# Kernel tuning notes

Hardware: AMD Instinct MI355X
Metric: run time of the kernel (lower is better)

Reference implementation:

```python
import jax, jax.numpy as jnp
import numpy as np

N = 8192
VOCAB = 32768
EMB = 128
HID = [128, 128]
NUM_CLASSES = 16
NUM_GRAPHS = 64


def setup_inputs() -> dict:
    key = jax.random.key(0)
    ks = jax.random.split(key, 10)
    x = jax.random.randint(ks[0], (N,), 0, VOCAB, dtype=jnp.int64 if jax.config.jax_enable_x64 else jnp.int32)
    m = jax.random.uniform(ks[1], (N, N), dtype=jnp.float32)  # dense weighted adjacency, positive degrees
    bm = (jnp.arange(N) * NUM_GRAPHS) // N  # sorted graph ids, every segment non-empty
    emb = jax.random.normal(ks[2], (VOCAB, EMB), dtype=jnp.float32)
    s1 = 1.0 / np.sqrt(EMB)
    w1 = jax.random.uniform(ks[3], (HID[0], EMB), jnp.float32, -s1, s1)
    b1 = jax.random.uniform(ks[4], (HID[0],), jnp.float32, -s1, s1)
    s2 = 1.0 / np.sqrt(HID[0])
    w2 = jax.random.uniform(ks[5], (HID[1], HID[0]), jnp.float32, -s2, s2)
    b2 = jax.random.uniform(ks[6], (HID[1],), jnp.float32, -s2, s2)
    sc = 1.0 / np.sqrt(HID[1])
    wc = jax.random.uniform(ks[7], (NUM_CLASSES, HID[1]), jnp.float32, -sc, sc)
    bc = jax.random.uniform(ks[8], (NUM_CLASSES,), jnp.float32, -sc, sc)
    return {"x": x, "m": m, "bm": bm, "emb": emb, "w1": w1, "b1": b1,
            "w2": w2, "b2": b2, "wc": wc, "bc": bc}


def _gcn_layer(h, m, w, b):
    # Linear -> ReLU (dropout=0 is identity)
    msg = jax.nn.relu(h @ w.T + b)
    row_deg = jnp.sum(m, axis=1, keepdims=True)   # (N,1)
    col_deg = jnp.sum(m, axis=0, keepdims=True)   # (1,N)
    deg = jnp.sqrt(row_deg) * jnp.sqrt(col_deg)   # rank-1 outer, same as mm(sqrt(rd), sqrt(cd))
    return (m / deg) @ msg                        # (N, out_dim)


def reference(x, m, bm, emb, w1, b1, w2, b2, wc, bc):
    h = emb[x]                                    # (N, EMB) embedding lookup
    h = _gcn_layer(h, m, w1, b1)
    h = _gcn_layer(h, m, w2, b2)
    pooled = jax.ops.segment_max(h, bm, num_segments=NUM_GRAPHS)  # (G, HID[-1]) max-pool per graph
    logits = pooled @ wc.T + bc                   # (G, NUM_CLASSES)
    return logits
```

## Files before the change

### kernel.cpp

```cpp
#include <hip/hip_runtime.h>
#include <stdint.h>


#define NN 8192
#define DH 128
#define NCLS 16
#define NGRAPH 64
#define SPLITK 8
#define KCHUNK (NN / SPLITK)

typedef float floatx4 __attribute__((ext_vector_type(4)));
typedef __bf16 bf16x8 __attribute__((ext_vector_type(8)));

__device__ __forceinline__ unsigned short f2bf_bits(float f) {
    union { float f; unsigned u; } v; v.f = f;
    unsigned u = v.u;
    u += 0x7fffu + ((u >> 16) & 1u);
    return (unsigned short)(u >> 16);
}

__device__ __forceinline__ void gload16(const void* g, void* l) {
    __builtin_amdgcn_global_load_lds(
        (const __attribute__((address_space(1))) void*)g,
        (__attribute__((address_space(3))) void*)l, 16, 0, 0);
}

__global__ __launch_bounds__(256) void k_zero(float* p, int n) {
    int i = blockIdx.x * 256 + threadIdx.x;
    if (i < n) p[i] = 0.f;
}

__global__ __launch_bounds__(256) void k_deg_cast(
    const float* __restrict__ m, unsigned short* __restrict__ mb,
    float* __restrict__ rd, float* __restrict__ cd)
{
    int rb = blockIdx.x >> 2;
    int cb = blockIdx.x & 3;
    int tid = threadIdx.x;
    int lane = tid & 63;
    int c = cb * 2048 + tid * 8;
    int r0 = rb * 32;
    float cs[8];
#pragma unroll
    for (int u = 0; u < 8; ++u) cs[u] = 0.f;
#pragma unroll 2
    for (int r = 0; r < 32; ++r) {
        int row = r0 + r;
        const float* p = m + (size_t)row * NN + c;
        float4 a = *(const float4*)p;
        float4 b = *(const float4*)(p + 4);
        cs[0] += a.x; cs[1] += a.y; cs[2] += a.z; cs[3] += a.w;
        cs[4] += b.x; cs[5] += b.y; cs[6] += b.z; cs[7] += b.w;
        float rs = ((a.x + a.y) + (a.z + a.w)) + ((b.x + b.y) + (b.z + b.w));
#pragma unroll
        for (int off = 1; off < 64; off <<= 1) rs += __shfl_xor(rs, off, 64);
        if (lane == 0) atomicAdd(&rd[row], rs);
        uint4 o;
        o.x = (unsigned)f2bf_bits(a.x) | ((unsigned)f2bf_bits(a.y) << 16);
        o.y = (unsigned)f2bf_bits(a.z) | ((unsigned)f2bf_bits(a.w) << 16);
        o.z = (unsigned)f2bf_bits(b.x) | ((unsigned)f2bf_bits(b.y) << 16);
        o.w = (unsigned)f2bf_bits(b.z) | ((unsigned)f2bf_bits(b.w) << 16);
        *(uint4*)(mb + (size_t)row * NN + c) = o;
    }
#pragma unroll
    for (int u = 0; u < 8; ++u) atomicAdd(&cd[c + u], cs[u]);
}

__global__ __launch_bounds__(256) void k_msg(
    const int* __restrict__ x, const float* __restrict__ emb,
    const float* __restrict__ part, const float* __restrict__ rdv,
    const float* __restrict__ w, const float* __restrict__ bias,
    const float* __restrict__ cdv, unsigned short* __restrict__ msgT,
    int layer)
{
    int tid = threadIdx.x;
    int wv = tid >> 6, lane = tid & 63;
    int quad = lane >> 4, r16 = lane & 15;
    int j = blockIdx.x * 64 + wv * 16 + r16;

    floatx4 acc[8];
#pragma unroll
    for (int t = 0; t < 8; ++t) acc[t] = (floatx4)0.f;

    const float* src;
    float presc = 1.f;
    if (layer == 1) {
        src = emb + (size_t)x[j] * DH;
    } else {
        src = part + (size_t)j * DH;
        presc = rsqrtf(rdv[j]);
    }

#pragma unroll
    for (int e0 = 0; e0 < DH; e0 += 32) {
        int ke = e0 + quad * 8;
        float v[8];
        if (layer == 1) {
            float4 a = *(const float4*)(src + ke);
            float4 b = *(const float4*)(src + ke + 4);
            v[0] = a.x; v[1] = a.y; v[2] = a.z; v[3] = a.w;
            v[4] = b.x; v[5] = b.y; v[6] = b.z; v[7] = b.w;
        } else {
#pragma unroll
            for (int u = 0; u < 8; ++u) v[u] = 0.f;
#pragma unroll
            for (int p2 = 0; p2 < SPLITK; ++p2) {
                const float* pp = src + (size_t)p2 * ((size_t)NN * DH) + ke;
                float4 a = *(const float4*)pp;
                float4 b = *(const float4*)(pp + 4);
                v[0] += a.x; v[1] += a.y; v[2] += a.z; v[3] += a.w;
                v[4] += b.x; v[5] += b.y; v[6] += b.z; v[7] += b.w;
            }
#pragma unroll
            for (int u = 0; u < 8; ++u) v[u] *= presc;
        }
        bf16x8 bf;
#pragma unroll
        for (int u = 0; u < 8; ++u) bf[u] = (__bf16)v[u];
#pragma unroll
        for (int t = 0; t < 8; ++t) {
            const float* wp = w + (size_t)(t * 16 + r16) * DH + ke;
            float4 wa = *(const float4*)wp;
            float4 wb = *(const float4*)(wp + 4);
            bf16x8 af;
            af[0] = (__bf16)wa.x; af[1] = (__bf16)wa.y; af[2] = (__bf16)wa.z; af[3] = (__bf16)wa.w;
            af[4] = (__bf16)wb.x; af[5] = (__bf16)wb.y; af[6] = (__bf16)wb.z; af[7] = (__bf16)wb.w;
            acc[t] = __builtin_amdgcn_mfma_f32_16x16x32_bf16(af, bf, acc[t], 0, 0, 0);
        }
    }
    float cs = rsqrtf(cdv[j]);
#pragma unroll
    for (int t = 0; t < 8; ++t) {
#pragma unroll
        for (int r = 0; r < 4; ++r) {
            int n = t * 16 + quad * 4 + r;
            float val = acc[t][r] + bias[n];
            val = fmaxf(val, 0.f) * cs;
            msgT[(size_t)n * NN + j] = f2bf_bits(val);
        }
    }
}

__global__ __launch_bounds__(256) void k_gemm(
    const unsigned short* __restrict__ A,
    const unsigned short* __restrict__ Bt,
    float* __restrict__ part)
{
    __shared__ unsigned short lA[128 * 32];
    __shared__ unsigned short lB[128 * 32];
    int mblk = blockIdx.x & 63;
    int kp = blockIdx.x >> 6;
    int tid = threadIdx.x;
    int wv = tid >> 6, lane = tid & 63;
    int quad = lane >> 4, r16 = lane & 15;
    int wm = wv >> 1, wn = wv & 1;
    size_t mbase = (size_t)mblk * 128;
    int kbase = kp * KCHUNK;

    floatx4 acc[4][4];
#pragma unroll
    for (int mi = 0; mi < 4; ++mi)
#pragma unroll
        for (int ni = 0; ni < 4; ++ni) acc[mi][ni] = (floatx4)0.f;

    int srow = lane >> 2;
    int kq = lane & 3;
    const unsigned short* gA = A + (mbase + wv * 32 + srow) * (size_t)NN + kbase + kq * 8;
    const unsigned short* gB = Bt + (size_t)(wv * 32 + srow) * NN + kbase + kq * 8;
    char* lAw = (char*)lA + wv * 2048;
    char* lBw = (char*)lB + wv * 2048;

    for (int it = 0; it < KCHUNK / 32; ++it) {
        gload16(gA, lAw);
        gload16(gA + (size_t)16 * NN, lAw + 1024);
        gload16(gB, lBw);
        gload16(gB + (size_t)16 * NN, lBw + 1024);
        __syncthreads();
        bf16x8 af[4], bf[4];
#pragma unroll
        for (int mi = 0; mi < 4; ++mi)
            af[mi] = *(const bf16x8*)((const char*)lA + ((wm * 64 + mi * 16 + r16) * 64 + quad * 16));
#pragma unroll
        for (int ni = 0; ni < 4; ++ni)
            bf[ni] = *(const bf16x8*)((const char*)lB + ((wn * 64 + ni * 16 + r16) * 64 + quad * 16));
#pragma unroll
        for (int mi = 0; mi < 4; ++mi)
#pragma unroll
            for (int ni = 0; ni < 4; ++ni)
                acc[mi][ni] = __builtin_amdgcn_mfma_f32_16x16x32_bf16(af[mi], bf[ni], acc[mi][ni], 0, 0, 0);
        __syncthreads();
        gA += 32; gB += 32;
    }

    float* outp = part + (size_t)kp * ((size_t)NN * DH);
#pragma unroll
    for (int mi = 0; mi < 4; ++mi) {
#pragma unroll
        for (int r = 0; r < 4; ++r) {
            size_t i = mbase + wm * 64 + mi * 16 + quad * 4 + r;
            float* op = outp + i * DH + wn * 64 + r16;
#pragma unroll
            for (int ni = 0; ni < 4; ++ni) op[ni * 16] = acc[mi][ni][r];
        }
    }
}

__global__ __launch_bounds__(256) void k_pool(
    const float* __restrict__ part, const float* __restrict__ rdv,
    const float* __restrict__ wc, const float* __restrict__ bc,
    float* __restrict__ out)
{
    __shared__ float red[256];
    __shared__ float pooled[128];
    int g = blockIdx.x;
    int tid = threadIdx.x;
    int c = tid & 127;
    int half = tid >> 7;
    float mx = -1e30f;
    for (int r = 0; r < 64; ++r) {
        int i = g * 128 + half * 64 + r;
        float s = 0.f;
#pragma unroll
        for (int p = 0; p < SPLITK; ++p)
            s += part[(size_t)p * ((size_t)NN * DH) + (size_t)i * DH + c];
        s *= rsqrtf(rdv[i]);
        mx = fmaxf(mx, s);
    }
    red[tid] = mx;
    __syncthreads();
    if (half == 0) pooled[c] = fmaxf(red[c], red[c + 128]);
    __syncthreads();
    if (tid < NCLS) {
        float a = bc[tid];
        const float* wr = wc + tid * 128;
#pragma unroll 8
        for (int k = 0; k < 128; ++k) a += pooled[k] * wr[k];
        out[g * NCLS + tid] = a;
    }
}

extern "C" void kernel_launch(void* const* d_in, const int* in_sizes, int n_in,
                              void* d_out, int out_size, void* d_ws, size_t ws_size,
                              hipStream_t stream)
{
    const int*   x   = (const int*)  d_in[0];
    const float* m   = (const float*)d_in[1];
    const float* emb = (const float*)d_in[3];
    const float* w1  = (const float*)d_in[4];
    const float* b1  = (const float*)d_in[5];
    const float* w2  = (const float*)d_in[6];
    const float* b2  = (const float*)d_in[7];
    const float* wc  = (const float*)d_in[8];
    const float* bc  = (const float*)d_in[9];
    float* out = (float*)d_out;

    char* ws = (char*)d_ws;
    unsigned short* mb = (unsigned short*)ws;
    float* rd  = (float*)(ws + (size_t)134217728);
    float* cd  = rd + NN;
    unsigned short* msgT = (unsigned short*)(cd + NN);
    float* part = (float*)((char*)msgT + (size_t)2 * NN * DH);

    k_zero<<<(2 * NN + 255) / 256, 256, 0, stream>>>(rd, 2 * NN);
    k_deg_cast<<<1024, 256, 0, stream>>>(m, mb, rd, cd);
    k_msg<<<NN / 64, 256, 0, stream>>>(x, emb, nullptr, nullptr, w1, b1, cd, msgT, 1);
    k_gemm<<<64 * SPLITK, 256, 0, stream>>>(mb, msgT, part);
    k_msg<<<NN / 64, 256, 0, stream>>>(nullptr, nullptr, part, rd, w2, b2, cd, msgT, 2);
    k_gemm<<<64 * SPLITK, 256, 0, stream>>>(mb, msgT, part);
    k_pool<<<NGRAPH, 256, 0, stream>>>(part, rd, wc, bc, out);
}
```

Before: 580.9 us.

## Split degree/cast kernel, drop LDS staging in GEMM, parallelize pooling

Replaces the fused degree+cast kernel, which used atomics, with three kernels: a row-per-wave cast that computes row sums directly, a column partial-sum pass over the bf16 copy, and a final column reduction. This removes the atomics and the zeroing kernel. The GEMM drops LDS staging and loads MFMA fragments straight from global memory, double-buffered in registers. Pooling is spread over 8x more blocks, with a separate small classify kernel. The extra pass over the 128MB bf16 matrix for column sums and the uncoalesced direct-global GEMM loads may add memory traffic, and column degrees are now summed from bf16-rounded values.

```diff
diff --git a/kernel.cpp b/kernel.cpp
--- a/kernel.cpp
+++ b/kernel.cpp
@@ -8,62 +8,75 @@
 #define NGRAPH 64
 #define SPLITK 8
 #define KCHUNK (NN / SPLITK)
+#define CDSLICE 256
 
 typedef float floatx4 __attribute__((ext_vector_type(4)));
 typedef __bf16 bf16x8 __attribute__((ext_vector_type(8)));
 
-__device__ __forceinline__ unsigned short f2bf_bits(float f) {
+__device__ __forceinline__ unsigned f2bf_bits(float f) {
     union { float f; unsigned u; } v; v.f = f;
     unsigned u = v.u;
     u += 0x7fffu + ((u >> 16) & 1u);
-    return (unsigned short)(u >> 16);
-}
-
-__device__ __forceinline__ void gload16(const void* g, void* l) {
-    __builtin_amdgcn_global_load_lds(
-        (const __attribute__((address_space(1))) void*)g,
-        (__attribute__((address_space(3))) void*)l, 16, 0, 0);
-}
-
-__global__ __launch_bounds__(256) void k_zero(float* p, int n) {
-    int i = blockIdx.x * 256 + threadIdx.x;
-    if (i < n) p[i] = 0.f;
-}
-
-__global__ __launch_bounds__(256) void k_deg_cast(
+    return u >> 16;
+}
+__device__ __forceinline__ float bf2f(unsigned bits16) {
+    union { unsigned u; float f; } v; v.u = bits16 << 16; return v.f;
+}
+
+__global__ __launch_bounds__(256) void k_cast(
     const float* __restrict__ m, unsigned short* __restrict__ mb,
-    float* __restrict__ rd, float* __restrict__ cd)
-{
-    int rb = blockIdx.x >> 2;
-    int cb = blockIdx.x & 3;
-    int tid = threadIdx.x;
-    int lane = tid & 63;
-    int c = cb * 2048 + tid * 8;
-    int r0 = rb * 32;
-    float cs[8];
-#pragma unroll
-    for (int u = 0; u < 8; ++u) cs[u] = 0.f;
-#pragma unroll 2
+    float* __restrict__ rd)
+{
+    int wv = threadIdx.x >> 6, lane = threadIdx.x & 63;
+    int row = blockIdx.x * 4 + wv;
+    const float* src = m + (size_t)row * NN;
+    unsigned short* dst = mb + (size_t)row * NN;
+    float rsum = 0.f;
+#pragma unroll 4
+    for (int it = 0; it < 32; ++it) {
+        int c = it * 256 + lane * 4;
+        float4 a = *(const float4*)(src + c);
+        rsum += (a.x + a.y) + (a.z + a.w);
+        uint2 o;
+        o.x = f2bf_bits(a.x) | (f2bf_bits(a.y) << 16);
+        o.y = f2bf_bits(a.z) | (f2bf_bits(a.w) << 16);
+        *(uint2*)(dst + c) = o;
+    }
+#pragma unroll
+    for (int off = 1; off < 64; off <<= 1) rsum += __shfl_xor(rsum, off, 64);
+    if (lane == 0) rd[row] = rsum;
+}
+
+__global__ __launch_bounds__(256) void k_cd(
+    const unsigned short* __restrict__ mb, float* __restrict__ cdpart)
+{
+    int cb = blockIdx.x & 3, rb = blockIdx.x >> 2;
+    int c = cb * 2048 + threadIdx.x * 8;
+    const unsigned short* p = mb + (size_t)rb * 32 * NN + c;
+    float s[8];
+#pragma unroll
+    for (int u = 0; u < 8; ++u) s[u] = 0.f;
+#pragma unroll 4
     for (int r = 0; r < 32; ++r) {
-        int row = r0 + r;
-        const float* p = m + (size_t)row * NN + c;
-        float4 a = *(const float4*)p;
-        float4 b = *(const float4*)(p + 4);
-        cs[0] += a.x; cs[1] += a.y; cs[2] += a.z; cs[3] += a.w;
-        cs[4] += b.x; cs[5] += b.y; cs[6] += b.z; cs[7] += b.w;
-        float rs = ((a.x + a.y) + (a.z + a.w)) + ((b.x + b.y) + (b.z + b.w));
-#pragma unroll
-        for (int off = 1; off < 64; off <<= 1) rs += __shfl_xor(rs, off, 64);
-        if (lane == 0) atomicAdd(&rd[row], rs);
-        uint4 o;
-        o.x = (unsigned)f2bf_bits(a.x) | ((unsigned)f2bf_bits(a.y) << 16);
-        o.y = (unsigned)f2bf_bits(a.z) | ((unsigned)f2bf_bits(a.w) << 16);
-        o.z = (unsigned)f2bf_bits(b.x) | ((unsigned)f2bf_bits(b.y) << 16);
-        o.w = (unsigned)f2bf_bits(b.z) | ((unsigned)f2bf_bits(b.w) << 16);
-        *(uint4*)(mb + (size_t)row * NN + c) = o;
-    }
-#pragma unroll
-    for (int u = 0; u < 8; ++u) atomicAdd(&cd[c + u], cs[u]);
+        uint4 v = *(const uint4*)(p + (size_t)r * NN);
+        s[0] += bf2f(v.x & 0xffffu); s[1] += bf2f(v.x >> 16);
+        s[2] += bf2f(v.y & 0xffffu); s[3] += bf2f(v.y >> 16);
+        s[4] += bf2f(v.z & 0xffffu); s[5] += bf2f(v.z >> 16);
+        s[6] += bf2f(v.w & 0xffffu); s[7] += bf2f(v.w >> 16);
+    }
+    float* op = cdpart + (size_t)rb * NN + c;
+    *(float4*)op = (float4){s[0], s[1], s[2], s[3]};
+    *(float4*)(op + 4) = (float4){s[4], s[5], s[6], s[7]};
+}
+
+__global__ __launch_bounds__(256) void k_cd2(
+    const float* __restrict__ cdpart, float* __restrict__ cd)
+{
+    int col = blockIdx.x * 256 + threadIdx.x;
+    float s = 0.f;
+#pragma unroll 8
+    for (int r = 0; r < CDSLICE; ++r) s += cdpart[(size_t)r * NN + col];
+    cd[col] = s;
 }
 
 __global__ __launch_bounds__(256) void k_msg(
@@ -136,7 +149,7 @@
             int n = t * 16 + quad * 4 + r;
             float val = acc[t][r] + bias[n];
             val = fmaxf(val, 0.f) * cs;
-            msgT[(size_t)n * NN + j] = f2bf_bits(val);
+            msgT[(size_t)n * NN + j] = (unsigned short)f2bf_bits(val);
         }
     }
 }
@@ -146,8 +159,6 @@
     const unsigned short* __restrict__ Bt,
     float* __restrict__ part)
 {
-    __shared__ unsigned short lA[128 * 32];
-    __shared__ unsigned short lB[128 * 32];
     int mblk = blockIdx.x & 63;
     int kp = blockIdx.x >> 6;
     int tid = threadIdx.x;
@@ -157,40 +168,44 @@
     size_t mbase = (size_t)mblk * 128;
     int kbase = kp * KCHUNK;
 
+    const unsigned short* a0 = A + (mbase + wm * 64 + r16) * (size_t)NN + kbase + quad * 8;
+    const unsigned short* b0 = Bt + (size_t)(wn * 64 + r16) * NN + kbase + quad * 8;
+
     floatx4 acc[4][4];
 #pragma unroll
     for (int mi = 0; mi < 4; ++mi)
 #pragma unroll
         for (int ni = 0; ni < 4; ++ni) acc[mi][ni] = (floatx4)0.f;
 
-    int srow = lane >> 2;
-    int kq = lane & 3;
-    const unsigned short* gA = A + (mbase + wv * 32 + srow) * (size_t)NN + kbase + kq * 8;
-    const unsigned short* gB = Bt + (size_t)(wv * 32 + srow) * NN + kbase + kq * 8;
-    char* lAw = (char*)lA + wv * 2048;
-    char* lBw = (char*)lB + wv * 2048;
-
-    for (int it = 0; it < KCHUNK / 32; ++it) {
-        gload16(gA, lAw);
-        gload16(gA + (size_t)16 * NN, lAw + 1024);
-        gload16(gB, lBw);
-        gload16(gB + (size_t)16 * NN, lBw + 1024);
-        __syncthreads();
-        bf16x8 af[4], bf[4];
-#pragma unroll
-        for (int mi = 0; mi < 4; ++mi)
-            af[mi] = *(const bf16x8*)((const char*)lA + ((wm * 64 + mi * 16 + r16) * 64 + quad * 16));
-#pragma unroll
-        for (int ni = 0; ni < 4; ++ni)
-            bf[ni] = *(const bf16x8*)((const char*)lB + ((wn * 64 + ni * 16 + r16) * 64 + quad * 16));
-#pragma unroll
-        for (int mi = 0; mi < 4; ++mi)
-#pragma unroll
-            for (int ni = 0; ni < 4; ++ni)
-                acc[mi][ni] = __builtin_amdgcn_mfma_f32_16x16x32_bf16(af[mi], bf[ni], acc[mi][ni], 0, 0, 0);
-        __syncthreads();
-        gA += 32; gB += 32;
-    }
+#define LOADF(AB, ks)                                                              \
+    do {                                                                           \
+        _Pragma("unroll")                                                          \
+        for (int q = 0; q < 4; ++q) {                                              \
+            AB##a[q] = *(const bf16x8*)(a0 + (size_t)q * 16 * NN + (ks) * 32);     \
+            AB##b[q] = *(const bf16x8*)(b0 + (size_t)q * 16 * NN + (ks) * 32);     \
+        }                                                                          \
+    } while (0)
+#define MFMAF(AB)                                                                  \
+    do {                                                                           \
+        _Pragma("unroll")                                                          \
+        for (int mi = 0; mi < 4; ++mi)                                             \
+            _Pragma("unroll")                                                      \
+            for (int ni = 0; ni < 4; ++ni)                                         \
+                acc[mi][ni] = __builtin_amdgcn_mfma_f32_16x16x32_bf16(             \
+                    AB##a[mi], AB##b[ni], acc[mi][ni], 0, 0, 0);                   \
+    } while (0)
+
+    bf16x8 pa[4], pb[4], qa[4], qb[4];
+    LOADF(p, 0);
+#pragma unroll
+    for (int ks = 0; ks < KCHUNK / 32; ks += 2) {
+        LOADF(q, ks + 1);
+        MFMAF(p);
+        if (ks + 2 < KCHUNK / 32) LOADF(p, ks + 2);
+        MFMAF(q);
+    }
+#undef LOADF
+#undef MFMAF
 
     float* outp = part + (size_t)kp * ((size_t)NN * DH);
 #pragma unroll
@@ -207,35 +222,44 @@
 
 __global__ __launch_bounds__(256) void k_pool(
     const float* __restrict__ part, const float* __restrict__ rdv,
-    const float* __restrict__ wc, const float* __restrict__ bc,
-    float* __restrict__ out)
+    float* __restrict__ pmax)
 {
     __shared__ float red[256];
-    __shared__ float pooled[128];
-    int g = blockIdx.x;
-    int tid = threadIdx.x;
-    int c = tid & 127;
-    int half = tid >> 7;
+    int g = blockIdx.x >> 3, rc = blockIdx.x & 7;
+    int c = threadIdx.x & 127, rh = threadIdx.x >> 7;
     float mx = -1e30f;
-    for (int r = 0; r < 64; ++r) {
-        int i = g * 128 + half * 64 + r;
+#pragma unroll
+    for (int r = 0; r < 8; ++r) {
+        int i = g * 128 + rc * 16 + rh * 8 + r;
         float s = 0.f;
 #pragma unroll
         for (int p = 0; p < SPLITK; ++p)
             s += part[(size_t)p * ((size_t)NN * DH) + (size_t)i * DH + c];
-        s *= rsqrtf(rdv[i]);
-        mx = fmaxf(mx, s);
-    }
-    red[tid] = mx;
+        mx = fmaxf(mx, s * rsqrtf(rdv[i]));
+    }
+    red[threadIdx.x] = mx;
     __syncthreads();
-    if (half == 0) pooled[c] = fmaxf(red[c], red[c + 128]);
+    if (rh == 0) pmax[(size_t)(g * 8 + rc) * 128 + c] = fmaxf(red[c], red[c + 128]);
+}
+
+__global__ __launch_bounds__(128) void k_classify(
+    const float* __restrict__ pmax, const float* __restrict__ wc,
+    const float* __restrict__ bc, float* __restrict__ out)
+{
+    __shared__ float pooled[128];
+    int g = blockIdx.x, t = threadIdx.x;
+    float mx = pmax[(size_t)(g * 8) * 128 + t];
+#pragma unroll
+    for (int rc = 1; rc < 8; ++rc)
+        mx = fmaxf(mx, pmax[(size_t)(g * 8 + rc) * 128 + t]);
+    pooled[t] = mx;
     __syncthreads();
-    if (tid < NCLS) {
-        float a = bc[tid];
-        const float* wr = wc + tid * 128;
+    if (t < NCLS) {
+        float a = bc[t];
+        const float* wr = wc + t * 128;
 #pragma unroll 8
         for (int k = 0; k < 128; ++k) a += pooled[k] * wr[k];
-        out[g * NCLS + tid] = a;
+        out[g * NCLS + t] = a;
     }
 }
 
@@ -256,16 +280,20 @@
 
     char* ws = (char*)d_ws;
     unsigned short* mb = (unsigned short*)ws;
-    float* rd  = (float*)(ws + (size_t)134217728);
-    float* cd  = rd + NN;
+    float* rd   = (float*)(ws + (size_t)134217728);
+    float* cd   = rd + NN;
     unsigned short* msgT = (unsigned short*)(cd + NN);
     float* part = (float*)((char*)msgT + (size_t)2 * NN * DH);
-
-    k_zero<<<(2 * NN + 255) / 256, 256, 0, stream>>>(rd, 2 * NN);
-    k_deg_cast<<<1024, 256, 0, stream>>>(m, mb, rd, cd);
+    float* cdpart = part;
+    float* pmax = part + (size_t)SPLITK * NN * DH;
+
+    k_cast<<<NN / 4, 256, 0, stream>>>(m, mb, rd);
+    k_cd<<<1024, 256, 0, stream>>>(mb, cdpart);
+    k_cd2<<<NN / 256, 256, 0, stream>>>(cdpart, cd);
     k_msg<<<NN / 64, 256, 0, stream>>>(x, emb, nullptr, nullptr, w1, b1, cd, msgT, 1);
     k_gemm<<<64 * SPLITK, 256, 0, stream>>>(mb, msgT, part);
     k_msg<<<NN / 64, 256, 0, stream>>>(nullptr, nullptr, part, rd, w2, b2, cd, msgT, 2);
     k_gemm<<<64 * SPLITK, 256, 0, stream>>>(mb, msgT, part);
-    k_pool<<<NGRAPH, 256, 0, stream>>>(part, rd, wc, bc, out);
-}
+    k_pool<<<NGRAPH * 8, 256, 0, stream>>>(part, rd, pmax);
+    k_classify<<<NGRAPH, 128, 0, stream>>>(pmax, wc, bc, out);
+}
```

After: 594.8 us. +2.4%, slower.
